# Kernel optimization log

Measured on AMD Instinct MI355X. Metric: run time of the kernel, lower is better.

## Reference

```python
import jax, jax.numpy as jnp
import numpy as np

B, N, DIM, H = 8, 1024, 1024, 16
D = DIM // H  # head dim = 64
SCALE = DIM ** (-0.5)  # NOTE: original uses full dim, not head dim


def setup_inputs() -> dict:
    key = jax.random.key(0)
    ks = jax.random.split(key, 8)
    x = jax.random.normal(ks[0], (B, N, DIM), dtype=jnp.float32)
    pos = jax.random.normal(ks[1], (B, N, DIM), dtype=jnp.float32)
    mask = jax.random.bernoulli(ks[2], 0.9, (B, N - 1))  # bool, [b, n-1]
    w_std = 0.02
    W_qk = jax.random.normal(ks[3], (2 * DIM, DIM), dtype=jnp.float32) * w_std  # Linear(dim, 2*dim_qk)
    W_v = jax.random.normal(ks[4], (DIM, DIM), dtype=jnp.float32) * w_std
    W_out = jax.random.normal(ks[5], (DIM, DIM), dtype=jnp.float32) * w_std
    b_out = jax.random.normal(ks[6], (DIM,), dtype=jnp.float32) * w_std
    return {"x": x, "mask": mask, "pos": pos, "W_qk": W_qk, "W_v": W_v,
            "W_out": W_out, "b_out": b_out}


def _split_heads(t):
    # b n (h d) -> b h n d
    b, n, _ = t.shape
    return t.reshape(b, n, H, D).transpose(0, 2, 1, 3)


def reference(x, mask, pos, W_qk, W_v, W_out, b_out):
    qk = x @ W_qk.T                       # [b, n, 2*dim]
    q, k = jnp.split(qk, 2, axis=-1)
    v = x @ W_v.T                         # [b, n, dim]
    q, k, v = _split_heads(q), _split_heads(k), _split_heads(v)  # [b,h,n,d]
    hpos = _split_heads(pos)
    q = q + hpos
    k = k + hpos
    dots = jnp.einsum('bhid,bhjd->bhij', q, k) * SCALE  # [b,h,n,n]
    mask_value = -jnp.finfo(dots.dtype).max
    # pad mask with True at position 0 (CLS token always visible)
    m = jnp.pad(mask, ((0, 0), (1, 0)), constant_values=True)  # [b, n]
    m2 = m[:, None, :] & m[:, :, None]                          # [b, n, n]
    dots = jnp.where(m2[:, None, :, :], dots, mask_value)
    attn = jax.nn.softmax(dots, axis=-1)
    out = jnp.einsum('bhij,bhjd->bhid', attn, v)  # [b,h,n,d]
    out = out.transpose(0, 2, 1, 3).reshape(x.shape[0], x.shape[1], DIM)  # b n (h d)
    out = out @ W_out.T + b_out  # dropout p=0.0 -> identity
    return out
```

## Files before the change

### kernel.cpp

```cpp
#include <hip/hip_runtime.h>


typedef unsigned short u16;
typedef short bf16x8 __attribute__((ext_vector_type(8)));
typedef float f32x4 __attribute__((ext_vector_type(4)));
typedef float f32x16 __attribute__((ext_vector_type(16)));

#define MFMA16(a, b, c) __builtin_amdgcn_mfma_f32_16x16x32_bf16((a), (b), (c), 0, 0, 0)
#define MFMA32(a, b, c) __builtin_amdgcn_mfma_f32_32x32x16_bf16((a), (b), (c), 0, 0, 0)

__device__ __forceinline__ u16 f2bf(float f) {
    union { float f; unsigned u; } x; x.f = f;
    unsigned r = x.u + 0x7fffu + ((x.u >> 16) & 1u);
    return (u16)(r >> 16);
}

__device__ __forceinline__ void gld16(const u16* g, u16* l) {
    __builtin_amdgcn_global_load_lds(
        (const __attribute__((address_space(1))) void*)g,
        (__attribute__((address_space(3))) void*)l, 16, 0, 0);
}

__global__ __launch_bounds__(256) void cast_all(
    const float* __restrict__ x, const float* __restrict__ wqk,
    const float* __restrict__ wv, const float* __restrict__ wout,
    u16* __restrict__ xbf, u16* __restrict__ wqkvbf, u16* __restrict__ woutbf) {
    int i = blockIdx.x * 256 + threadIdx.x;
    const float* src; u16* dst; int off;
    if (i < 2097152)      { src = x;    dst = xbf;              off = i; }
    else if (i < 2621440) { src = wqk;  dst = wqkvbf;           off = i - 2097152; }
    else if (i < 2883584) { src = wv;   dst = wqkvbf + 2097152; off = i - 2621440; }
    else                  { src = wout; dst = woutbf;           off = i - 2883584; }
    float4 v = ((const float4*)src)[off];
    ushort4 o;
    o.x = f2bf(v.x); o.y = f2bf(v.y); o.z = f2bf(v.z); o.w = f2bf(v.w);
    ((ushort4*)dst)[off] = o;
}

__global__ __launch_bounds__(256) void gemm_qk(
    const u16* __restrict__ A,
    const u16* __restrict__ Bw,
    const float* __restrict__ pos,
    u16* __restrict__ Q, u16* __restrict__ Kx) {
    const int n0 = blockIdx.x * 128, m0 = blockIdx.y * 128;
    const int t = threadIdx.x, w = t >> 6, ln = t & 63;
    const int l15 = ln & 15, l4 = ln >> 4;
    const int wm = (w >> 1) * 64, wn = (w & 1) * 64;

    __shared__ u16 As[128 * 64];
    __shared__ u16 Bs[128 * 64];

    f32x4 acc[4][4];
#pragma unroll
    for (int i = 0; i < 4; ++i)
#pragma unroll
        for (int j = 0; j < 4; ++j) acc[i][j] = (f32x4){0.f, 0.f, 0.f, 0.f};

    const int sr = ln >> 3;
    const int scx = ((ln & 7) ^ sr) * 8;
    const int x0 = (l15 & 7);
    for (int k0 = 0; k0 < 1024; k0 += 64) {
        __syncthreads();
#pragma unroll
        for (int p = 0; p < 4; ++p) {
            int rbase = w * 32 + p * 8;
            gld16(A  + (size_t)(m0 + rbase + sr) * 1024 + k0 + scx, &As[rbase * 64]);
            gld16(Bw + (size_t)(n0 + rbase + sr) * 1024 + k0 + scx, &Bs[rbase * 64]);
        }
        __syncthreads();
#pragma unroll
        for (int kt = 0; kt < 2; ++kt) {
            bf16x8 a[4], bfr[4];
#pragma unroll
            for (int mt = 0; mt < 4; ++mt)
                a[mt] = *(const bf16x8*)&As[(wm + mt * 16 + l15) * 64 + ((kt * 4 + l4) ^ x0) * 8];
#pragma unroll
            for (int nt = 0; nt < 4; ++nt)
                bfr[nt] = *(const bf16x8*)&Bs[(wn + nt * 16 + l15) * 64 + ((kt * 4 + l4) ^ x0) * 8];
#pragma unroll
            for (int mt = 0; mt < 4; ++mt)
#pragma unroll
                for (int nt = 0; nt < 4; ++nt)
                    acc[mt][nt] = MFMA16(a[mt], bfr[nt], acc[mt][nt]);
        }
    }
#pragma unroll
    for (int mt = 0; mt < 4; ++mt)
#pragma unroll
        for (int nt = 0; nt < 4; ++nt)
#pragma unroll
            for (int r = 0; r < 4; ++r) {
                int i = m0 + wm + mt * 16 + l4 * 4 + r;
                int j = n0 + wn + nt * 16 + l15;
                int bb = i >> 10, n = i & 1023;
                int jj = j & 1023;
                float v = acc[mt][nt][r] + pos[(size_t)i * 1024 + jj];
                int hh = jj >> 6, dd = jj & 63;
                size_t idx = (((size_t)(bb * 16 + hh)) * 1024 + n) * 64 + dd;
                if (j < 1024) Q[idx] = f2bf(v * 0.045084220027780106f);
                else          Kx[idx] = f2bf(v);
            }
}

__global__ __launch_bounds__(256) void zero_k(
    const int* __restrict__ maskIn,
    u16* __restrict__ Kx) {
    int tid = blockIdx.x * 256 + threadIdx.x;
    int seg = tid & 7;
    int row = tid >> 3;
    int n = row & 1023;
    int b = row >> 14;
    if (n == 0) return;
    if (maskIn[b * 1023 + n - 1] != 0) return;
    uint4 z = {0u, 0u, 0u, 0u};
    *(uint4*)(Kx + (size_t)row * 64 + seg * 8) = z;
}

__global__ __launch_bounds__(256) void gemm_v(
    const u16* __restrict__ Wv,
    const u16* __restrict__ X,
    u16* __restrict__ Vt) {
    const int n0 = blockIdx.x * 128, m0 = blockIdx.y * 128;
    const int bIdx = blockIdx.z;
    const u16* Xb = X + (size_t)bIdx * 1048576;
    const int t = threadIdx.x, w = t >> 6, ln = t & 63;
    const int l15 = ln & 15, l4 = ln >> 4;
    const int wm = (w >> 1) * 64, wn = (w & 1) * 64;

    __shared__ u16 As[128 * 64];
    __shared__ u16 Bs[128 * 64];

    f32x4 acc[4][4];
#pragma unroll
    for (int i = 0; i < 4; ++i)
#pragma unroll
        for (int j = 0; j < 4; ++j) acc[i][j] = (f32x4){0.f, 0.f, 0.f, 0.f};

    const int sr = ln >> 3;
    const int scx = ((ln & 7) ^ sr) * 8;
    const int x0 = (l15 & 7);
    for (int k0 = 0; k0 < 1024; k0 += 64) {
        __syncthreads();
#pragma unroll
        for (int p = 0; p < 4; ++p) {
            int rbase = w * 32 + p * 8;
            gld16(Wv + (size_t)(m0 + rbase + sr) * 1024 + k0 + scx, &As[rbase * 64]);
            gld16(Xb + (size_t)(n0 + rbase + sr) * 1024 + k0 + scx, &Bs[rbase * 64]);
        }
        __syncthreads();
#pragma unroll
        for (int kt = 0; kt < 2; ++kt) {
            bf16x8 a[4], bfr[4];
#pragma unroll
            for (int mt = 0; mt < 4; ++mt)
                a[mt] = *(const bf16x8*)&As[(wm + mt * 16 + l15) * 64 + ((kt * 4 + l4) ^ x0) * 8];
#pragma unroll
            for (int nt = 0; nt < 4; ++nt)
                bfr[nt] = *(const bf16x8*)&Bs[(wn + nt * 16 + l15) * 64 + ((kt * 4 + l4) ^ x0) * 8];
#pragma unroll
            for (int mt = 0; mt < 4; ++mt)
#pragma unroll
                for (int nt = 0; nt < 4; ++nt)
                    acc[mt][nt] = MFMA16(a[mt], bfr[nt], acc[mt][nt]);
        }
    }
#pragma unroll
    for (int mt = 0; mt < 4; ++mt)
#pragma unroll
        for (int nt = 0; nt < 4; ++nt)
#pragma unroll
            for (int r = 0; r < 4; ++r) {
                int i = m0 + wm + mt * 16 + l4 * 4 + r;
                int j = n0 + wn + nt * 16 + l15;
                Vt[((size_t)(bIdx * 1024 + i)) * 1024 + j] = f2bf(acc[mt][nt][r]);
            }
}

__global__ __launch_bounds__(64) void vsum_kernel(const u16* __restrict__ Vt,
                                                  const int* __restrict__ maskIn,
                                                  float* __restrict__ Vsum,
                                                  float* __restrict__ Vmask) {
    int row = blockIdx.x, ln = threadIdx.x;
    int b = row >> 10;
    const u16* p = Vt + (size_t)row * 1024 + ln * 16;
    uint4 a = *(const uint4*)p;
    uint4 bq = *(const uint4*)(p + 8);
    float s = 0.f, sm = 0.f;
    unsigned vv[8] = {a.x, a.y, a.z, a.w, bq.x, bq.y, bq.z, bq.w};
#pragma unroll
    for (int i = 0; i < 8; ++i) {
        int j0 = ln * 16 + 2 * i;
        float lo = __uint_as_float(vv[i] << 16);
        float hi = __uint_as_float(vv[i] & 0xffff0000u);
        s += lo + hi;
        bool ok0 = (j0 == 0) || (maskIn[b * 1023 + j0 - 1] != 0);
        bool ok1 = (maskIn[b * 1023 + j0] != 0);
        if (!ok0) sm += lo;
        if (!ok1) sm += hi;
    }
#pragma unroll
    for (int d = 1; d < 64; d <<= 1) { s += __shfl_xor(s, d); sm += __shfl_xor(sm, d); }
    if (ln == 0) { Vsum[row] = s; Vmask[row] = sm; }
}

__global__ __launch_bounds__(512) void attn_kernel(
    const u16* __restrict__ Q,
    const u16* __restrict__ Kx,
    const u16* __restrict__ Vt,
    const int* __restrict__ maskIn,
    const float* __restrict__ Vsum,
    const float* __restrict__ Vmask,
    u16* __restrict__ O) {
    const int gid = blockIdx.x;
    const int bh = gid & 127;
    const int qt = gid >> 7;
    const int b = bh >> 4, h = bh & 15;
    const int t = threadIdx.x, w = t >> 6, ln = t & 63;
    const int half = w >> 2, wq = w & 3;
    const int l31 = ln & 31, l5 = ln >> 5;

    __shared__ __align__(16) char lds[36896];
    u16* Ks = (u16*)(lds + half * 18432);
    u16* Vs = (u16*)(lds + half * 18432 + 9216);
    float* nm = (float*)(lds + 36864);

    {
        float cnt = 0.f;
        for (int i = t; i < 1023; i += 512)
            cnt += (maskIn[b * 1023 + i] == 0) ? 1.f : 0.f;
#pragma unroll
        for (int d = 1; d < 64; d <<= 1) cnt += __shfl_xor(cnt, d);
        if (ln == 0) nm[w] = cnt;
    }

    const size_t qkbase = (size_t)bh * 65536;
    const int q0 = qt * 128 + wq * 32;
    const int q = q0 + l31;

    bf16x8 bq[4];
#pragma unroll
    for (int kt = 0; kt < 4; ++kt)
        bq[kt] = *(const bf16x8*)(Q + qkbase + (size_t)q * 64 + kt * 16 + l5 * 8);

    float lsum = 0.f;
    f32x16 o0 = {0,0,0,0,0,0,0,0,0,0,0,0,0,0,0,0};
    f32x16 o1 = {0,0,0,0,0,0,0,0,0,0,0,0,0,0,0,0};

    const int th = t & 255;
    const int srow = th >> 2, sc = (th & 3) * 16;
    const int jbase = half * 512;

    for (int jt = 0; jt < 8; ++jt) {
        const int j0 = jbase + jt * 64;
        __syncthreads();
        {
            uint4 kv  = *(const uint4*)(Kx + qkbase + (size_t)(j0 + srow) * 64 + sc);
            uint4 kv2 = *(const uint4*)(Kx + qkbase + (size_t)(j0 + srow) * 64 + sc + 8);
            *(uint4*)&Ks[srow * 72 + sc] = kv;
            *(uint4*)&Ks[srow * 72 + sc + 8] = kv2;
            uint4 vv  = *(const uint4*)(Vt + qkbase + (size_t)srow * 1024 + j0 + sc);
            uint4 vv2 = *(const uint4*)(Vt + qkbase + (size_t)srow * 1024 + j0 + sc + 8);
            *(uint4*)&Vs[srow * 72 + sc] = vv;
            *(uint4*)&Vs[srow * 72 + sc + 8] = vv2;
        }
        __syncthreads();

        f32x16 st0 = {0,0,0,0,0,0,0,0,0,0,0,0,0,0,0,0};
        f32x16 st1 = {0,0,0,0,0,0,0,0,0,0,0,0,0,0,0,0};
#pragma unroll
        for (int ktk = 0; ktk < 4; ++ktk) {
            bf16x8 ak0 = *(const bf16x8*)&Ks[(l31) * 72 + ktk * 16 + l5 * 8];
            bf16x8 ak1 = *(const bf16x8*)&Ks[(32 + l31) * 72 + ktk * 16 + l5 * 8];
            st0 = MFMA32(ak0, bq[ktk], st0);
            st1 = MFMA32(ak1, bq[ktk], st1);
        }
#pragma unroll
        for (int i = 0; i < 16; ++i) {
            float p0 = __builtin_amdgcn_exp2f(st0[i]);
            float p1 = __builtin_amdgcn_exp2f(st1[i]);
            st0[i] = p0;
            st1[i] = p1;
            lsum += p0 + p1;
        }
        unsigned pk0[8], pk1[8];
#pragma unroll
        for (int g = 0; g < 4; ++g) {
#pragma unroll
            for (int qq = 0; qq < 2; ++qq) {
                unsigned a0 = __float_as_uint(st0[g * 4 + 2 * qq]) + 0x8000u;
                unsigned a1 = __float_as_uint(st0[g * 4 + 2 * qq + 1]) + 0x8000u;
                pk0[2 * g + qq] = (a1 & 0xffff0000u) | (a0 >> 16);
                unsigned c0 = __float_as_uint(st1[g * 4 + 2 * qq]) + 0x8000u;
                unsigned c1 = __float_as_uint(st1[g * 4 + 2 * qq + 1]) + 0x8000u;
                pk1[2 * g + qq] = (c1 & 0xffff0000u) | (c0 >> 16);
            }
        }
        bf16x8 pf[4];
#pragma unroll
        for (int kt = 0; kt < 4; ++kt) {
            const int hh = kt & 1;
            unsigned own0, own1, off0, off1;
            if (kt < 2) {
                own0 = l5 ? pk0[4 * hh + 2] : pk0[4 * hh];
                own1 = l5 ? pk0[4 * hh + 3] : pk0[4 * hh + 1];
                off0 = l5 ? pk0[4 * hh]     : pk0[4 * hh + 2];
                off1 = l5 ? pk0[4 * hh + 1] : pk0[4 * hh + 3];
            } else {
                own0 = l5 ? pk1[4 * hh + 2] : pk1[4 * hh];
                own1 = l5 ? pk1[4 * hh + 3] : pk1[4 * hh + 1];
                off0 = l5 ? pk1[4 * hh]     : pk1[4 * hh + 2];
                off1 = l5 ? pk1[4 * hh + 1] : pk1[4 * hh + 3];
            }
            unsigned ex0 = (unsigned)__shfl_xor((int)off0, 32);
            unsigned ex1 = (unsigned)__shfl_xor((int)off1, 32);
            unsigned dw0 = l5 ? ex0 : own0;
            unsigned dw1 = l5 ? ex1 : own1;
            unsigned dw2 = l5 ? own0 : ex0;
            unsigned dw3 = l5 ? own1 : ex1;
            union { unsigned u[4]; bf16x8 v; } cv;
            cv.u[0] = dw0; cv.u[1] = dw1; cv.u[2] = dw2; cv.u[3] = dw3;
            pf[kt] = cv.v;
        }
#pragma unroll
        for (int kt = 0; kt < 4; ++kt) {
            bf16x8 av0 = *(const bf16x8*)&Vs[(l31) * 72 + kt * 16 + l5 * 8];
            bf16x8 av1 = *(const bf16x8*)&Vs[(32 + l31) * 72 + kt * 16 + l5 * 8];
            o0 = MFMA32(av0, pf[kt], o0);
            o1 = MFMA32(av1, pf[kt], o1);
        }
    }
    __syncthreads();
    float* comb = (float*)lds;
    if (half == 1) {
        float* dst = comb + ((size_t)(wq * 64 + ln)) * 33;
#pragma unroll
        for (int i = 0; i < 16; ++i) { dst[i] = o0[i]; dst[16 + i] = o1[i]; }
        dst[32] = lsum;
    }
    __syncthreads();
    if (half == 0) {
        const float* src = comb + ((size_t)(wq * 64 + ln)) * 33;
#pragma unroll
        for (int i = 0; i < 16; ++i) { o0[i] += src[i]; o1[i] += src[16 + i]; }
        lsum += src[32];
        float lrow = lsum + __shfl_xor(lsum, 32);
        float nmaskb = nm[0] + nm[1] + nm[2] + nm[3] + nm[4] + nm[5] + nm[6] + nm[7];
        lrow -= nmaskb;
        const float linv = 1.f / lrow;
        const int n = q0 + l31;
        const bool rqv = (n == 0) || (maskIn[b * 1023 + n - 1] != 0);
        u16* orow = O + ((size_t)(b * 1024 + n)) * 1024 + h * 64;
#pragma unroll
        for (int g = 0; g < 4; ++g) {
            ushort4 s0, s1;
            unsigned short* p0 = (unsigned short*)&s0;
            unsigned short* p1 = (unsigned short*)&s1;
#pragma unroll
            for (int r = 0; r < 4; ++r) {
                int reg = 4 * g + r;
                int d0 = 8 * g + 4 * l5 + r;
                float v0 = rqv ? (o0[reg] - Vmask[bh * 64 + d0]) * linv
                               : Vsum[bh * 64 + d0] * 0.0009765625f;
                float v1 = rqv ? (o1[reg] - Vmask[bh * 64 + 32 + d0]) * linv
                               : Vsum[bh * 64 + 32 + d0] * 0.0009765625f;
                p0[r] = f2bf(v0);
                p1[r] = f2bf(v1);
            }
            *(ushort4*)&orow[8 * g + 4 * l5] = s0;
            *(ushort4*)&orow[32 + 8 * g + 4 * l5] = s1;
        }
    }
}

__global__ __launch_bounds__(256) void gemm_out(
    const u16* __restrict__ A,
    const u16* __restrict__ Bw,
    const float* __restrict__ bias,
    float* __restrict__ out) {
    const int n0 = blockIdx.x * 128, m0 = blockIdx.y * 128;
    const int t = threadIdx.x, w = t >> 6, ln = t & 63;
    const int l15 = ln & 15, l4 = ln >> 4;
    const int wm = (w >> 1) * 64, wn = (w & 1) * 64;

    __shared__ u16 As[128 * 64];
    __shared__ u16 Bs[128 * 64];

    f32x4 acc[4][4];
#pragma unroll
    for (int i = 0; i < 4; ++i)
#pragma unroll
        for (int j = 0; j < 4; ++j) acc[i][j] = (f32x4){0.f, 0.f, 0.f, 0.f};

    const int sr = ln >> 3;
    const int scx = ((ln & 7) ^ sr) * 8;
    const int x0 = (l15 & 7);
    for (int k0 = 0; k0 < 1024; k0 += 64) {
        __syncthreads();
#pragma unroll
        for (int p = 0; p < 4; ++p) {
            int rbase = w * 32 + p * 8;
            gld16(A  + (size_t)(m0 + rbase + sr) * 1024 + k0 + scx, &As[rbase * 64]);
            gld16(Bw + (size_t)(n0 + rbase + sr) * 1024 + k0 + scx, &Bs[rbase * 64]);
        }
        __syncthreads();
#pragma unroll
        for (int kt = 0; kt < 2; ++kt) {
            bf16x8 a[4], bfr[4];
#pragma unroll
            for (int mt = 0; mt < 4; ++mt)
                a[mt] = *(const bf16x8*)&As[(wm + mt * 16 + l15) * 64 + ((kt * 4 + l4) ^ x0) * 8];
#pragma unroll
            for (int nt = 0; nt < 4; ++nt)
                bfr[nt] = *(const bf16x8*)&Bs[(wn + nt * 16 + l15) * 64 + ((kt * 4 + l4) ^ x0) * 8];
#pragma unroll
            for (int mt = 0; mt < 4; ++mt)
#pragma unroll
                for (int nt = 0; nt < 4; ++nt)
                    acc[mt][nt] = MFMA16(a[mt], bfr[nt], acc[mt][nt]);
        }
    }
#pragma unroll
    for (int mt = 0; mt < 4; ++mt)
#pragma unroll
        for (int nt = 0; nt < 4; ++nt)
#pragma unroll
            for (int r = 0; r < 4; ++r) {
                int i = m0 + wm + mt * 16 + l4 * 4 + r;
                int j = n0 + wn + nt * 16 + l15;
                out[(size_t)i * 1024 + j] = acc[mt][nt][r] + bias[j];
            }
}

extern "C" void kernel_launch(void* const* d_in, const int* in_sizes, int n_in,
                              void* d_out, int out_size, void* d_ws, size_t ws_size,
                              hipStream_t stream) {
    const float* x    = (const float*)d_in[0];
    const int*   mask = (const int*)d_in[1];
    const float* pos  = (const float*)d_in[2];
    const float* wqk  = (const float*)d_in[3];
    const float* wv   = (const float*)d_in[4];
    const float* wout = (const float*)d_in[5];
    const float* bout = (const float*)d_in[6];

    char* ws = (char*)d_ws;
    u16* xbf    = (u16*)(ws + 0);
    u16* wqkvbf = (u16*)(ws + 16777216);
    u16* woutbf = (u16*)(ws + 23068672);
    u16* Qb     = (u16*)(ws + 25165824);
    u16* Kb     = (u16*)(ws + 41943040);
    u16* Vtb    = (u16*)(ws + 58720256);
    float* Vsum = (float*)(ws + 16777216);
    float* Vmask = (float*)(ws + 16777216 + 32768);

    cast_all<<<12288, 256, 0, stream>>>(x, wqk, wv, wout, xbf, wqkvbf, woutbf);

    gemm_qk<<<dim3(16, 64), 256, 0, stream>>>(xbf, wqkvbf, pos, Qb, Kb);
    zero_k<<<4096, 256, 0, stream>>>(mask, Kb);
    gemm_v<<<dim3(8, 8, 8), 256, 0, stream>>>(wqkvbf + 2097152, xbf, Vtb);
    vsum_kernel<<<8192, 64, 0, stream>>>(Vtb, mask, Vsum, Vmask);
    attn_kernel<<<1024, 512, 0, stream>>>(Qb, Kb, Vtb, mask, Vsum, Vmask, xbf);
    gemm_out<<<dim3(8, 64), 256, 0, stream>>>(xbf, woutbf, bout, (float*)d_out);
}
```

Before: 296.4 us.

## Double-buffer K/V tiles with async global-to-LDS loads and XOR swizzle

Replaces the synchronous register-staged K/V tile loads with global_load_lds DMA into a double-buffered LDS region, prefetching the next 64-key tile while the current one is computed. The padded row stride is replaced by an XOR swizzle to avoid bank conflicts, and s_setprio raises priority around MFMA blocks. LDS per block grows from about 36KB to 64KB, which may reduce occupancy, and correctness depends on the manual vmcnt waits and barriers.

```diff
diff --git a/kernel.cpp b/kernel.cpp
--- a/kernel.cpp
+++ b/kernel.cpp
@@ -219,10 +219,8 @@
     const int half = w >> 2, wq = w & 3;
     const int l31 = ln & 31, l5 = ln >> 5;
 
-    __shared__ __align__(16) char lds[36896];
-    u16* Ks = (u16*)(lds + half * 18432);
-    u16* Vs = (u16*)(lds + half * 18432 + 9216);
-    float* nm = (float*)(lds + 36864);
+    __shared__ __align__(16) char lds[65568];
+    float* nm = (float*)(lds + 65536);
 
     {
         float cnt = 0.f;
@@ -246,34 +244,51 @@
     f32x16 o0 = {0,0,0,0,0,0,0,0,0,0,0,0,0,0,0,0};
     f32x16 o1 = {0,0,0,0,0,0,0,0,0,0,0,0,0,0,0,0};
 
-    const int th = t & 255;
-    const int srow = th >> 2, sc = (th & 3) * 16;
     const int jbase = half * 512;
-
+    const int srow = ln >> 3;
+    const int swz8 = (ln & 7) ^ srow;
+    u16* ldsH = (u16*)(lds + half * 32768);
+    const int rb = wq * 16;
+
+#define ATTN_STAGE(c, j0_)                                                              \
+    do {                                                                                \
+        gld16(Kx + qkbase + (size_t)((j0_) + rb + srow) * 64 + swz8 * 8,                \
+              ldsH + (c) * 8192 + rb * 64);                                             \
+        gld16(Kx + qkbase + (size_t)((j0_) + rb + 8 + srow) * 64 + swz8 * 8,            \
+              ldsH + (c) * 8192 + (rb + 8) * 64);                                       \
+        gld16(Vt + qkbase + (size_t)(rb + srow) * 1024 + (j0_) + swz8 * 8,              \
+              ldsH + (c) * 8192 + 4096 + rb * 64);                                      \
+        gld16(Vt + qkbase + (size_t)(rb + 8 + srow) * 1024 + (j0_) + swz8 * 8,          \
+              ldsH + (c) * 8192 + 4096 + (rb + 8) * 64);                                \
+    } while (0)
+
+    ATTN_STAGE(0, jbase);
+    int cur = 0;
     for (int jt = 0; jt < 8; ++jt) {
         const int j0 = jbase + jt * 64;
-        __syncthreads();
-        {
-            uint4 kv  = *(const uint4*)(Kx + qkbase + (size_t)(j0 + srow) * 64 + sc);
-            uint4 kv2 = *(const uint4*)(Kx + qkbase + (size_t)(j0 + srow) * 64 + sc + 8);
-            *(uint4*)&Ks[srow * 72 + sc] = kv;
-            *(uint4*)&Ks[srow * 72 + sc + 8] = kv2;
-            uint4 vv  = *(const uint4*)(Vt + qkbase + (size_t)srow * 1024 + j0 + sc);
-            uint4 vv2 = *(const uint4*)(Vt + qkbase + (size_t)srow * 1024 + j0 + sc + 8);
-            *(uint4*)&Vs[srow * 72 + sc] = vv;
-            *(uint4*)&Vs[srow * 72 + sc + 8] = vv2;
-        }
-        __syncthreads();
+        if (jt < 7) {
+            ATTN_STAGE(cur ^ 1, j0 + 64);
+            asm volatile("s_waitcnt vmcnt(4)" ::: "memory");
+        } else {
+            asm volatile("s_waitcnt vmcnt(0)" ::: "memory");
+        }
+        __builtin_amdgcn_s_barrier();
+
+        const u16* Kb = ldsH + cur * 8192;
+        const u16* Vb = Kb + 4096;
 
         f32x16 st0 = {0,0,0,0,0,0,0,0,0,0,0,0,0,0,0,0};
         f32x16 st1 = {0,0,0,0,0,0,0,0,0,0,0,0,0,0,0,0};
+        __builtin_amdgcn_s_setprio(1);
 #pragma unroll
         for (int ktk = 0; ktk < 4; ++ktk) {
-            bf16x8 ak0 = *(const bf16x8*)&Ks[(l31) * 72 + ktk * 16 + l5 * 8];
-            bf16x8 ak1 = *(const bf16x8*)&Ks[(32 + l31) * 72 + ktk * 16 + l5 * 8];
+            const int sw = ((ktk * 2 + l5) ^ (l31 & 7)) * 8;
+            bf16x8 ak0 = *(const bf16x8*)&Kb[l31 * 64 + sw];
+            bf16x8 ak1 = *(const bf16x8*)&Kb[(32 + l31) * 64 + sw];
             st0 = MFMA32(ak0, bq[ktk], st0);
             st1 = MFMA32(ak1, bq[ktk], st1);
         }
+        __builtin_amdgcn_s_setprio(0);
 #pragma unroll
         for (int i = 0; i < 16; ++i) {
             float p0 = __builtin_amdgcn_exp2f(st0[i]);
@@ -321,15 +336,22 @@
             cv.u[0] = dw0; cv.u[1] = dw1; cv.u[2] = dw2; cv.u[3] = dw3;
             pf[kt] = cv.v;
         }
+        __builtin_amdgcn_s_setprio(1);
 #pragma unroll
         for (int kt = 0; kt < 4; ++kt) {
-            bf16x8 av0 = *(const bf16x8*)&Vs[(l31) * 72 + kt * 16 + l5 * 8];
-            bf16x8 av1 = *(const bf16x8*)&Vs[(32 + l31) * 72 + kt * 16 + l5 * 8];
+            const int sw = ((kt * 2 + l5) ^ (l31 & 7)) * 8;
+            bf16x8 av0 = *(const bf16x8*)&Vb[l31 * 64 + sw];
+            bf16x8 av1 = *(const bf16x8*)&Vb[(32 + l31) * 64 + sw];
             o0 = MFMA32(av0, pf[kt], o0);
             o1 = MFMA32(av1, pf[kt], o1);
         }
-    }
-    __syncthreads();
+        __builtin_amdgcn_s_setprio(0);
+        __builtin_amdgcn_sched_barrier(0);
+        __builtin_amdgcn_s_barrier();
+        cur ^= 1;
+    }
+#undef ATTN_STAGE
+
     float* comb = (float*)lds;
     if (half == 1) {
         float* dst = comb + ((size_t)(wq * 64 + ln)) * 33;
```

New measurement: 294.6 us. No clear change (-0.6%).
